# Optimization experiments

Measured on AMD Instinct MI355X. Metric: run time of the kernel, lower is better.

The kernel has to match this reference:

```python
import jax, jax.numpy as jnp
import numpy as np

N, NQ, M, DQ, DK, DV, H = 4, 512, 512, 256, 256, 256, 256


def setup_inputs() -> dict:
    key = jax.random.key(0)
    ks = jax.random.split(key, 6)
    scale_q = 1.0 / np.sqrt(DQ)
    scale_k = 1.0 / np.sqrt(DK)
    scale_v = 1.0 / np.sqrt(H)
    return {
        "query": jax.random.normal(ks[0], (N, NQ, DQ), jnp.float32),
        "key": jax.random.normal(ks[1], (N, M, DK), jnp.float32),
        "value": jax.random.normal(ks[2], (N, M, DV), jnp.float32),
        "W_q": jax.random.normal(ks[3], (DQ, H), jnp.float32) * scale_q,
        "W_k": jax.random.normal(ks[4], (DK, H), jnp.float32) * scale_k,
        "W_v": jax.random.normal(ks[5], (H,), jnp.float32) * scale_v,
    }


def reference(query, key, value, W_q, W_k, W_v):
    # project: (N, n, H) and (N, m, H)
    q = jnp.einsum("bnd,dh->bnh", query, W_q)
    k = jnp.einsum("bmd,dh->bmh", key, W_k)
    # broadcast add -> (N, n, m, H), tanh, project H->1 -> scores (N, n, m)
    scores = jnp.einsum("bnmh,h->bnm", jnp.tanh(q[:, :, None, :] + k[:, None, :, :]), W_v)
    attn = jax.nn.softmax(scores, axis=-1)  # (N, n, m)
    return jnp.einsum("bnm,bmv->bnv", attn, value)
```

## Files before the change

### kernel.cpp

```cpp
#include <hip/hip_runtime.h>

#define NB 4
#define NQL 512
#define ML 512
#define DDIM 256
#define HDIM 256

static constexpr float TWO_LOG2E = 2.8853900817779268f;
static constexpr float LOG2E     = 1.4426950408889634f;

#define PJX(j, c, Wr)                                   \
    acc[0][0] = fmaf(XA[j].c, Wr[j].x, acc[0][0]);      \
    acc[0][1] = fmaf(XA[j].c, Wr[j].y, acc[0][1]);      \
    acc[0][2] = fmaf(XA[j].c, Wr[j].z, acc[0][2]);      \
    acc[0][3] = fmaf(XA[j].c, Wr[j].w, acc[0][3]);      \
    acc[1][0] = fmaf(XB[j].c, Wr[j].x, acc[1][0]);      \
    acc[1][1] = fmaf(XB[j].c, Wr[j].y, acc[1][1]);      \
    acc[1][2] = fmaf(XB[j].c, Wr[j].z, acc[1][2]);      \
    acc[1][3] = fmaf(XB[j].c, Wr[j].w, acc[1][3]);
#define PJ_STEP(j) { PJX(j, x, W0) PJX(j, y, W1) PJX(j, z, W2) PJX(j, w, W3) }

__global__ __launch_bounds__(512) void proj_kernel(
    const float* __restrict__ q_src, const float* __restrict__ k_src,
    const float* __restrict__ Wq,    const float* __restrict__ Wk,
    float* __restrict__ EqT,         float* __restrict__ EkT)
{
    const int idx   = blockIdx.x;
    const int b     = idx & 3;
    const int which = (idx >> 2) & 1;
    const int lt    = (idx >> 3) & 7;
    const int ht    = idx >> 6;
    const float* __restrict__ src = which ? k_src : q_src;
    const float* __restrict__ W   = which ? Wk : Wq;
    float* __restrict__ outT      = which ? EkT : EqT;

    const int l0 = lt * 64, h0 = ht * 64;
    const int t  = threadIdx.x;
    const int tx = t & 15;
    const int ty = t >> 4;

    const float* xr0 = &src[(size_t)(b * NQL + l0 + ty * 2) * DDIM];
    const float* xr1 = xr0 + DDIM;
    const float* wc  = &W[h0 + tx * 4];

    float4 XA[4], XB[4], W0[4], W1[4], W2[4], W3[4];
    #pragma unroll
    for (int j = 0; j < 4; ++j) {
        XA[j] = *(const float4*)(xr0 + j * 4);
        XB[j] = *(const float4*)(xr1 + j * 4);
        const float* wr = wc + (size_t)(j * 4) * HDIM;
        W0[j] = *(const float4*)(wr);
        W1[j] = *(const float4*)(wr + HDIM);
        W2[j] = *(const float4*)(wr + 2 * HDIM);
        W3[j] = *(const float4*)(wr + 3 * HDIM);
    }
    float acc[2][4] = {};

    for (int g = 0; g < 15; ++g) {
        #pragma unroll
        for (int j = 0; j < 4; ++j) {
            PJ_STEP(j)
            const int dc = 4 * g + j + 4;
            XA[j] = *(const float4*)(xr0 + dc * 4);
            XB[j] = *(const float4*)(xr1 + dc * 4);
            const float* wr = wc + (size_t)(dc * 4) * HDIM;
            W0[j] = *(const float4*)(wr);
            W1[j] = *(const float4*)(wr + HDIM);
            W2[j] = *(const float4*)(wr + 2 * HDIM);
            W3[j] = *(const float4*)(wr + 3 * HDIM);
        }
    }
    #pragma unroll
    for (int j = 0; j < 4; ++j) { PJ_STEP(j) }

    #pragma unroll
    for (int j = 0; j < 4; ++j) {
        float2 o;
        o.x = __builtin_amdgcn_exp2f(acc[0][j] * TWO_LOG2E);
        o.y = __builtin_amdgcn_exp2f(acc[1][j] * TWO_LOG2E);
        *(float2*)&outT[(size_t)(b * HDIM + h0 + tx * 4 + j) * NQL + l0 + ty * 2] = o;
    }
}

#define SC_STEP(j, wv)                                       \
    {                                                        \
        swv += (wv);                                         \
        const float nw2 = -2.0f * (wv);                      \
        float a00 = fmaf(QV[j].x, KV[j].x, 1.0f);            \
        float a01 = fmaf(QV[j].x, KV[j].y, 1.0f);            \
        float a02 = fmaf(QV[j].x, KV[j].z, 1.0f);            \
        float a03 = fmaf(QV[j].x, KV[j].w, 1.0f);            \
        float a10 = fmaf(QV[j].y, KV[j].x, 1.0f);            \
        float a11 = fmaf(QV[j].y, KV[j].y, 1.0f);            \
        float a12 = fmaf(QV[j].y, KV[j].z, 1.0f);            \
        float a13 = fmaf(QV[j].y, KV[j].w, 1.0f);            \
        float r0 = __builtin_amdgcn_rcpf(a00 * a01);         \
        float r1 = __builtin_amdgcn_rcpf(a02 * a03);         \
        float r2 = __builtin_amdgcn_rcpf(a10 * a11);         \
        float r3 = __builtin_amdgcn_rcpf(a12 * a13);         \
        float t0 = nw2 * r0, t1 = nw2 * r1;                  \
        float t2 = nw2 * r2, t3 = nw2 * r3;                  \
        acc0[0] = fmaf(t0, a01, acc0[0]);                    \
        acc0[1] = fmaf(t0, a00, acc0[1]);                    \
        acc0[2] = fmaf(t1, a03, acc0[2]);                    \
        acc0[3] = fmaf(t1, a02, acc0[3]);                    \
        acc1[0] = fmaf(t2, a11, acc1[0]);                    \
        acc1[1] = fmaf(t2, a10, acc1[1]);                    \
        acc1[2] = fmaf(t3, a13, acc1[2]);                    \
        acc1[3] = fmaf(t3, a12, acc1[3]);                    \
    }

__global__ __launch_bounds__(512) void scores_kernel(
    const float* __restrict__ EqT, const float* __restrict__ EkT,
    const float* __restrict__ Wv, float* __restrict__ P,
    float* __restrict__ Spart)
{
    const int idx = blockIdx.x;
    const int b   = idx & 3;
    const int mt  = (idx >> 2) & 3;
    const int nt  = idx >> 4;
    const int m0  = mt * 128, n0 = nt * 32;
    const int t   = threadIdx.x;
    const int tx  = t & 31;
    const int ty  = t >> 5;

    const float* qbase = &EqT[(size_t)b * HDIM * NQL + n0 + ty * 2];
    const float* kbase = &EkT[(size_t)b * HDIM * ML + m0 + tx * 4];

    float2 QV[8];
    float4 KV[8];
    float  WB[8];
    #pragma unroll
    for (int j = 0; j < 8; ++j) {
        QV[j] = *(const float2*)(qbase + (size_t)j * NQL);
        KV[j] = *(const float4*)(kbase + (size_t)j * ML);
        WB[j] = Wv[j];
    }

    float acc0[4] = {}, acc1[4] = {};
    float swv = 0.f;

    for (int g = 0; g < 31; ++g) {
        const float* qn = qbase + (size_t)(8 * g + 8) * NQL;
        const float* kn = kbase + (size_t)(8 * g + 8) * ML;
        #pragma unroll
        for (int j = 0; j < 8; ++j) {
            SC_STEP(j, WB[j])
            QV[j] = *(const float2*)(qn + (size_t)j * NQL);
            KV[j] = *(const float4*)(kn + (size_t)j * ML);
            WB[j] = Wv[8 * g + 8 + j];
        }
    }
    #pragma unroll
    for (int j = 0; j < 8; ++j) { SC_STEP(j, WB[j]) }

    float rs[2];
    {
        float4 p;
        p.x = __builtin_amdgcn_exp2f((swv + acc0[0]) * LOG2E);
        p.y = __builtin_amdgcn_exp2f((swv + acc0[1]) * LOG2E);
        p.z = __builtin_amdgcn_exp2f((swv + acc0[2]) * LOG2E);
        p.w = __builtin_amdgcn_exp2f((swv + acc0[3]) * LOG2E);
        *(float4*)&P[(size_t)(b * NQL + n0 + ty * 2 + 0) * ML + m0 + tx * 4] = p;
        rs[0] = (p.x + p.y) + (p.z + p.w);
    }
    {
        float4 p;
        p.x = __builtin_amdgcn_exp2f((swv + acc1[0]) * LOG2E);
        p.y = __builtin_amdgcn_exp2f((swv + acc1[1]) * LOG2E);
        p.z = __builtin_amdgcn_exp2f((swv + acc1[2]) * LOG2E);
        p.w = __builtin_amdgcn_exp2f((swv + acc1[3]) * LOG2E);
        *(float4*)&P[(size_t)(b * NQL + n0 + ty * 2 + 1) * ML + m0 + tx * 4] = p;
        rs[1] = (p.x + p.y) + (p.z + p.w);
    }
    #pragma unroll
    for (int off = 1; off < 32; off <<= 1) {
        rs[0] += __shfl_xor(rs[0], off);
        rs[1] += __shfl_xor(rs[1], off);
    }
    if (tx == 0) {
        float2 o = {rs[0], rs[1]};
        *(float2*)&Spart[(size_t)(mt * NB + b) * NQL + n0 + ty * 2] = o;
    }
}

#define AV_ONE(j, i, r, comp)                                        \
    acc[i][0] = fmaf(PS[j][i].comp, VS[j][r].x, acc[i][0]);          \
    acc[i][1] = fmaf(PS[j][i].comp, VS[j][r].y, acc[i][1]);          \
    acc[i][2] = fmaf(PS[j][i].comp, VS[j][r].z, acc[i][2]);          \
    acc[i][3] = fmaf(PS[j][i].comp, VS[j][r].w, acc[i][3]);
#define AV_R(j, r, comp) \
    AV_ONE(j, 0, r, comp) AV_ONE(j, 1, r, comp) AV_ONE(j, 2, r, comp) AV_ONE(j, 3, r, comp)
#define AV_STEP(j) AV_R(j, 0, x) AV_R(j, 1, y) AV_R(j, 2, z) AV_R(j, 3, w)

__global__ __launch_bounds__(256) void av_kernel(
    const float* __restrict__ P, const float* __restrict__ Spart,
    const float* __restrict__ V, float* __restrict__ O)
{
    const int idx = blockIdx.x;
    const int b   = idx & 3;
    const int vt  = (idx >> 2) & 3;
    const int nt  = idx >> 4;
    const int v0  = vt * 64, n0 = nt * 16;
    const int t    = threadIdx.x;
    const int lane = t & 63;
    const int wid  = t >> 6;
    const int tx   = lane & 15;
    const int tn   = lane >> 4;

    __shared__ float sInv[16];
    __shared__ float sRed[3][16][64];

    if (t < 16) {
        float s = 0.f;
        #pragma unroll
        for (int mt = 0; mt < 4; ++mt)
            s += Spart[(size_t)(mt * NB + b) * NQL + n0 + t];
        sInv[t] = 1.0f / s;
    }

    const float* pbase = &P[(size_t)(b * NQL + n0 + tn * 4) * ML + wid * 128];
    const float* vbase = &V[(size_t)(b * ML + wid * 128) * DDIM + v0 + tx * 4];

    float4 PS[4][4], VS[4][4];
    #pragma unroll
    for (int j = 0; j < 4; ++j) {
        #pragma unroll
        for (int r = 0; r < 4; ++r) {
            PS[j][r] = *(const float4*)(pbase + (size_t)r * ML + j * 4);
            VS[j][r] = *(const float4*)(vbase + (size_t)(j * 4 + r) * DDIM);
        }
    }
    float acc[4][4] = {};

    for (int g = 0; g < 7; ++g) {
        #pragma unroll
        for (int j = 0; j < 4; ++j) {
            AV_STEP(j)
            const int mc = 4 * g + j + 4;
            #pragma unroll
            for (int r = 0; r < 4; ++r) {
                PS[j][r] = *(const float4*)(pbase + (size_t)r * ML + mc * 4);
                VS[j][r] = *(const float4*)(vbase + (size_t)(mc * 4 + r) * DDIM);
            }
        }
    }
    #pragma unroll
    for (int j = 0; j < 4; ++j) { AV_STEP(j) }

    __syncthreads();
    if (wid != 0) {
        #pragma unroll
        for (int i = 0; i < 4; ++i) {
            float4 r = {acc[i][0], acc[i][1], acc[i][2], acc[i][3]};
            *(float4*)&sRed[wid - 1][tn * 4 + i][tx * 4] = r;
        }
    }
    __syncthreads();
    if (wid == 0) {
        #pragma unroll
        for (int i = 0; i < 4; ++i) {
            float4 r1 = *(const float4*)&sRed[0][tn * 4 + i][tx * 4];
            float4 r2 = *(const float4*)&sRed[1][tn * 4 + i][tx * 4];
            float4 r3 = *(const float4*)&sRed[2][tn * 4 + i][tx * 4];
            const float inv = sInv[tn * 4 + i];
            float4 o;
            o.x = (acc[i][0] + r1.x + r2.x + r3.x) * inv;
            o.y = (acc[i][1] + r1.y + r2.y + r3.y) * inv;
            o.z = (acc[i][2] + r1.z + r2.z + r3.z) * inv;
            o.w = (acc[i][3] + r1.w + r2.w + r3.w) * inv;
            *(float4*)&O[(size_t)(b * NQL + n0 + tn * 4 + i) * DDIM + v0 + tx * 4] = o;
        }
    }
}

extern "C" void kernel_launch(void* const* d_in, const int* in_sizes, int n_in,
                              void* d_out, int out_size, void* d_ws, size_t ws_size,
                              hipStream_t stream)
{
    const float* query = (const float*)d_in[0];
    const float* key   = (const float*)d_in[1];
    const float* value = (const float*)d_in[2];
    const float* Wq    = (const float*)d_in[3];
    const float* Wk    = (const float*)d_in[4];
    const float* Wv    = (const float*)d_in[5];
    float* out = (float*)d_out;

    float* EqT   = (float*)d_ws;
    float* EkT   = EqT + (size_t)NB * HDIM * NQL;
    float* P     = EkT + (size_t)NB * HDIM * ML;
    float* Spart = P + (size_t)NB * NQL * ML;

    proj_kernel<<<dim3(256), 512, 0, stream>>>(query, key, Wq, Wk, EqT, EkT);
    scores_kernel<<<dim3(256), 512, 0, stream>>>(EqT, EkT, Wv, P, Spart);
    av_kernel<<<dim3(512), 256, 0, stream>>>(P, Spart, value, out);
}
```

Measured before the change: 149.6 us.

## Replace deep register prefetch with double-buffered loads fenced by sched barriers

```diff
diff --git a/kernel.cpp b/kernel.cpp
--- a/kernel.cpp
+++ b/kernel.cpp
@@ -9,16 +9,39 @@
 static constexpr float TWO_LOG2E = 2.8853900817779268f;
 static constexpr float LOG2E     = 1.4426950408889634f;
 
-#define PJX(j, c, Wr)                                   \
-    acc[0][0] = fmaf(XA[j].c, Wr[j].x, acc[0][0]);      \
-    acc[0][1] = fmaf(XA[j].c, Wr[j].y, acc[0][1]);      \
-    acc[0][2] = fmaf(XA[j].c, Wr[j].z, acc[0][2]);      \
-    acc[0][3] = fmaf(XA[j].c, Wr[j].w, acc[0][3]);      \
-    acc[1][0] = fmaf(XB[j].c, Wr[j].x, acc[1][0]);      \
-    acc[1][1] = fmaf(XB[j].c, Wr[j].y, acc[1][1]);      \
-    acc[1][2] = fmaf(XB[j].c, Wr[j].z, acc[1][2]);      \
-    acc[1][3] = fmaf(XB[j].c, Wr[j].w, acc[1][3]);
-#define PJ_STEP(j) { PJX(j, x, W0) PJX(j, y, W1) PJX(j, z, W2) PJX(j, w, W3) }
+#define SB() __builtin_amdgcn_sched_barrier(0)
+
+#define PJC(xs0, xs1, wv)                              \
+    acc[0][0] = fmaf(xs0, (wv).x, acc[0][0]);          \
+    acc[0][1] = fmaf(xs0, (wv).y, acc[0][1]);          \
+    acc[0][2] = fmaf(xs0, (wv).z, acc[0][2]);          \
+    acc[0][3] = fmaf(xs0, (wv).w, acc[0][3]);          \
+    acc[1][0] = fmaf(xs1, (wv).x, acc[1][0]);          \
+    acc[1][1] = fmaf(xs1, (wv).y, acc[1][1]);          \
+    acc[1][2] = fmaf(xs1, (wv).z, acc[1][2]);          \
+    acc[1][3] = fmaf(xs1, (wv).w, acc[1][3]);
+
+#define PJ_LOAD(X0, X1, Wr, c)                                         \
+    {                                                                  \
+        const int d0_ = (c) * 8;                                       \
+        X0[0] = *(const float4*)(xr0 + d0_);                           \
+        X0[1] = *(const float4*)(xr0 + d0_ + 4);                       \
+        X1[0] = *(const float4*)(xr1 + d0_);                           \
+        X1[1] = *(const float4*)(xr1 + d0_ + 4);                       \
+        _Pragma("unroll")                                              \
+        for (int r_ = 0; r_ < 8; ++r_)                                 \
+            Wr[r_] = *(const float4*)(wc + (size_t)(d0_ + r_) * HDIM); \
+    }
+
+#define PJ_COMP(X0, X1, Wr)                        \
+    PJC(X0[0].x, X1[0].x, Wr[0])                   \
+    PJC(X0[0].y, X1[0].y, Wr[1])                   \
+    PJC(X0[0].z, X1[0].z, Wr[2])                   \
+    PJC(X0[0].w, X1[0].w, Wr[3])                   \
+    PJC(X0[1].x, X1[1].x, Wr[4])                   \
+    PJC(X0[1].y, X1[1].y, Wr[5])                   \
+    PJC(X0[1].z, X1[1].z, Wr[6])                   \
+    PJC(X0[1].w, X1[1].w, Wr[7])
 
 __global__ __launch_bounds__(512) void proj_kernel(
     const float* __restrict__ q_src, const float* __restrict__ k_src,
@@ -43,35 +66,27 @@
     const float* xr1 = xr0 + DDIM;
     const float* wc  = &W[h0 + tx * 4];
 
-    float4 XA[4], XB[4], W0[4], W1[4], W2[4], W3[4];
-    #pragma unroll
-    for (int j = 0; j < 4; ++j) {
-        XA[j] = *(const float4*)(xr0 + j * 4);
-        XB[j] = *(const float4*)(xr1 + j * 4);
-        const float* wr = wc + (size_t)(j * 4) * HDIM;
-        W0[j] = *(const float4*)(wr);
-        W1[j] = *(const float4*)(wr + HDIM);
-        W2[j] = *(const float4*)(wr + 2 * HDIM);
-        W3[j] = *(const float4*)(wr + 3 * HDIM);
-    }
+    float4 XA0[2], XA1[2], WA[8];
+    float4 XB0[2], XB1[2], WB[8];
     float acc[2][4] = {};
 
-    for (int g = 0; g < 15; ++g) {
-        #pragma unroll
-        for (int j = 0; j < 4; ++j) {
-            PJ_STEP(j)
-            const int dc = 4 * g + j + 4;
-            XA[j] = *(const float4*)(xr0 + dc * 4);
-            XB[j] = *(const float4*)(xr1 + dc * 4);
-            const float* wr = wc + (size_t)(dc * 4) * HDIM;
-            W0[j] = *(const float4*)(wr);
-            W1[j] = *(const float4*)(wr + HDIM);
-            W2[j] = *(const float4*)(wr + 2 * HDIM);
-            W3[j] = *(const float4*)(wr + 3 * HDIM);
-        }
-    }
-    #pragma unroll
-    for (int j = 0; j < 4; ++j) { PJ_STEP(j) }
+    PJ_LOAD(XA0, XA1, WA, 0)
+    SB();
+    for (int v = 0; v < 15; ++v) {
+        PJ_LOAD(XB0, XB1, WB, 2 * v + 1)
+        SB();
+        PJ_COMP(XA0, XA1, WA)
+        SB();
+        PJ_LOAD(XA0, XA1, WA, 2 * v + 2)
+        SB();
+        PJ_COMP(XB0, XB1, WB)
+        SB();
+    }
+    PJ_LOAD(XB0, XB1, WB, 31)
+    SB();
+    PJ_COMP(XA0, XA1, WA)
+    SB();
+    PJ_COMP(XB0, XB1, WB)
 
     #pragma unroll
     for (int j = 0; j < 4; ++j) {
@@ -82,18 +97,18 @@
     }
 }
 
-#define SC_STEP(j, wv)                                       \
+#define SC_EVAL(Q, K, j, wv)                                 \
     {                                                        \
         swv += (wv);                                         \
         const float nw2 = -2.0f * (wv);                      \
-        float a00 = fmaf(QV[j].x, KV[j].x, 1.0f);            \
-        float a01 = fmaf(QV[j].x, KV[j].y, 1.0f);            \
-        float a02 = fmaf(QV[j].x, KV[j].z, 1.0f);            \
-        float a03 = fmaf(QV[j].x, KV[j].w, 1.0f);            \
-        float a10 = fmaf(QV[j].y, KV[j].x, 1.0f);            \
-        float a11 = fmaf(QV[j].y, KV[j].y, 1.0f);            \
-        float a12 = fmaf(QV[j].y, KV[j].z, 1.0f);            \
-        float a13 = fmaf(QV[j].y, KV[j].w, 1.0f);            \
+        float a00 = fmaf(Q[j].x, K[j].x, 1.0f);              \
+        float a01 = fmaf(Q[j].x, K[j].y, 1.0f);              \
+        float a02 = fmaf(Q[j].x, K[j].z, 1.0f);              \
+        float a03 = fmaf(Q[j].x, K[j].w, 1.0f);              \
+        float a10 = fmaf(Q[j].y, K[j].x, 1.0f);              \
+        float a11 = fmaf(Q[j].y, K[j].y, 1.0f);              \
+        float a12 = fmaf(Q[j].y, K[j].z, 1.0f);              \
+        float a13 = fmaf(Q[j].y, K[j].w, 1.0f);              \
         float r0 = __builtin_amdgcn_rcpf(a00 * a01);         \
         float r1 = __builtin_amdgcn_rcpf(a02 * a03);         \
         float r2 = __builtin_amdgcn_rcpf(a10 * a11);         \
@@ -110,6 +125,21 @@
         acc1[3] = fmaf(t3, a12, acc1[3]);                    \
     }
 
+#define SC_LOAD(Q, K, Wb, c)                                           \
+    {                                                                  \
+        const int h0_ = (c) * 4;                                       \
+        _Pragma("unroll")                                              \
+        for (int j_ = 0; j_ < 4; ++j_) {                               \
+            Q[j_]  = *(const float2*)(qbase + (size_t)(h0_ + j_) * NQL); \
+            K[j_]  = *(const float4*)(kbase + (size_t)(h0_ + j_) * ML);  \
+            Wb[j_] = Wv[h0_ + j_];                                     \
+        }                                                              \
+    }
+
+#define SC_COMP(Q, K, Wb)                                              \
+    { SC_EVAL(Q, K, 0, Wb[0]) SC_EVAL(Q, K, 1, Wb[1])                  \
+      SC_EVAL(Q, K, 2, Wb[2]) SC_EVAL(Q, K, 3, Wb[3]) }
+
 __global__ __launch_bounds__(512) void scores_kernel(
     const float* __restrict__ EqT, const float* __restrict__ EkT,
     const float* __restrict__ Wv, float* __restrict__ P,
@@ -127,32 +157,29 @@
     const float* qbase = &EqT[(size_t)b * HDIM * NQL + n0 + ty * 2];
     const float* kbase = &EkT[(size_t)b * HDIM * ML + m0 + tx * 4];
 
-    float2 QV[8];
-    float4 KV[8];
-    float  WB[8];
-    #pragma unroll
-    for (int j = 0; j < 8; ++j) {
-        QV[j] = *(const float2*)(qbase + (size_t)j * NQL);
-        KV[j] = *(const float4*)(kbase + (size_t)j * ML);
-        WB[j] = Wv[j];
-    }
-
+    float2 QA[4], QB[4];
+    float4 KA[4], KB[4];
+    float  WA[4], WB[4];
     float acc0[4] = {}, acc1[4] = {};
     float swv = 0.f;
 
-    for (int g = 0; g < 31; ++g) {
-        const float* qn = qbase + (size_t)(8 * g + 8) * NQL;
-        const float* kn = kbase + (size_t)(8 * g + 8) * ML;
-        #pragma unroll
-        for (int j = 0; j < 8; ++j) {
-            SC_STEP(j, WB[j])
-            QV[j] = *(const float2*)(qn + (size_t)j * NQL);
-            KV[j] = *(const float4*)(kn + (size_t)j * ML);
-            WB[j] = Wv[8 * g + 8 + j];
-        }
-    }
-    #pragma unroll
-    for (int j = 0; j < 8; ++j) { SC_STEP(j, WB[j]) }
+    SC_LOAD(QA, KA, WA, 0)
+    SB();
+    for (int v = 0; v < 31; ++v) {
+        SC_LOAD(QB, KB, WB, 2 * v + 1)
+        SB();
+        SC_COMP(QA, KA, WA)
+        SB();
+        SC_LOAD(QA, KA, WA, 2 * v + 2)
+        SB();
+        SC_COMP(QB, KB, WB)
+        SB();
+    }
+    SC_LOAD(QB, KB, WB, 63)
+    SB();
+    SC_COMP(QA, KA, WA)
+    SB();
+    SC_COMP(QB, KB, WB)
 
     float rs[2];
     {
@@ -184,14 +211,27 @@
     }
 }
 
-#define AV_ONE(j, i, r, comp)                                        \
-    acc[i][0] = fmaf(PS[j][i].comp, VS[j][r].x, acc[i][0]);          \
-    acc[i][1] = fmaf(PS[j][i].comp, VS[j][r].y, acc[i][1]);          \
-    acc[i][2] = fmaf(PS[j][i].comp, VS[j][r].z, acc[i][2]);          \
-    acc[i][3] = fmaf(PS[j][i].comp, VS[j][r].w, acc[i][3]);
-#define AV_R(j, r, comp) \
-    AV_ONE(j, 0, r, comp) AV_ONE(j, 1, r, comp) AV_ONE(j, 2, r, comp) AV_ONE(j, 3, r, comp)
-#define AV_STEP(j) AV_R(j, 0, x) AV_R(j, 1, y) AV_R(j, 2, z) AV_R(j, 3, w)
+#define AV_ONE(PSb, VSb, i, r, comp)                                 \
+    acc[i][0] = fmaf(PSb[i].comp, VSb[r].x, acc[i][0]);              \
+    acc[i][1] = fmaf(PSb[i].comp, VSb[r].y, acc[i][1]);              \
+    acc[i][2] = fmaf(PSb[i].comp, VSb[r].z, acc[i][2]);              \
+    acc[i][3] = fmaf(PSb[i].comp, VSb[r].w, acc[i][3]);
+#define AV_RR(PSb, VSb, r, comp)                                     \
+    AV_ONE(PSb, VSb, 0, r, comp) AV_ONE(PSb, VSb, 1, r, comp)        \
+    AV_ONE(PSb, VSb, 2, r, comp) AV_ONE(PSb, VSb, 3, r, comp)
+#define AV_COMP(PSb, VSb)                                            \
+    AV_RR(PSb, VSb, 0, x) AV_RR(PSb, VSb, 1, y)                      \
+    AV_RR(PSb, VSb, 2, z) AV_RR(PSb, VSb, 3, w)
+
+#define AV_LOAD(PSb, VSb, c)                                              \
+    {                                                                     \
+        const int mm_ = (c) * 4;                                          \
+        _Pragma("unroll")                                                 \
+        for (int r_ = 0; r_ < 4; ++r_) {                                  \
+            PSb[r_] = *(const float4*)(pbase + (size_t)r_ * ML + mm_);    \
+            VSb[r_] = *(const float4*)(vbase + (size_t)(mm_ + r_) * DDIM);\
+        }                                                                 \
+    }
 
 __global__ __launch_bounds__(256) void av_kernel(
     const float* __restrict__ P, const float* __restrict__ Spart,
@@ -222,31 +262,27 @@
     const float* pbase = &P[(size_t)(b * NQL + n0 + tn * 4) * ML + wid * 128];
     const float* vbase = &V[(size_t)(b * ML + wid * 128) * DDIM + v0 + tx * 4];
 
-    float4 PS[4][4], VS[4][4];
-    #pragma unroll
-    for (int j = 0; j < 4; ++j) {
-        #pragma unroll
-        for (int r = 0; r < 4; ++r) {
-            PS[j][r] = *(const float4*)(pbase + (size_t)r * ML + j * 4);
-            VS[j][r] = *(const float4*)(vbase + (size_t)(j * 4 + r) * DDIM);
-        }
-    }
+    float4 PA[4], VA[4];
+    float4 PB[4], VB[4];
     float acc[4][4] = {};
 
-    for (int g = 0; g < 7; ++g) {
-        #pragma unroll
-        for (int j = 0; j < 4; ++j) {
-            AV_STEP(j)
-            const int mc = 4 * g + j + 4;
-            #pragma unroll
-            for (int r = 0; r < 4; ++r) {
-                PS[j][r] = *(const float4*)(pbase + (size_t)r * ML + mc * 4);
-                VS[j][r] = *(const float4*)(vbase + (size_t)(mc * 4 + r) * DDIM);
-            }
-        }
-    }
-    #pragma unroll
-    for (int j = 0; j < 4; ++j) { AV_STEP(j) }
+    AV_LOAD(PA, VA, 0)
+    SB();
+    for (int v = 0; v < 15; ++v) {
+        AV_LOAD(PB, VB, 2 * v + 1)
+        SB();
+        AV_COMP(PA, VA)
+        SB();
+        AV_LOAD(PA, VA, 2 * v + 2)
+        SB();
+        AV_COMP(PB, VB)
+        SB();
+    }
+    AV_LOAD(PB, VB, 31)
+    SB();
+    AV_COMP(PA, VA)
+    SB();
+    AV_COMP(PB, VB)
 
     __syncthreads();
     if (wid != 0) {
```

Measured after the change: 143.6 us. 4.0% less time.
